# Kernel optimization log

Hardware: AMD Instinct MI355X
Metric: run time of the kernel (lower is better)

Reference implementation:

```python
import jax, jax.numpy as jnp
import numpy as np

B, D_IN, NQ, D_OUT = 65536, 1024, 64, 1024
PI = float(np.pi)


def setup_inputs() -> dict:
    key = jax.random.key(0)
    ks = jax.random.split(key, 6)
    return {
        "x": jax.random.normal(ks[0], (B, D_IN), dtype=jnp.float32),
        "W_in": jax.random.normal(ks[1], (NQ, D_IN), dtype=jnp.float32) * 0.02,
        "b_in": jax.random.normal(ks[2], (NQ,), dtype=jnp.float32) * 0.02,
        "quantum_params": jax.random.normal(ks[3], (NQ, 3), dtype=jnp.float32) * 0.1,
        "W_out": jax.random.normal(ks[4], (D_OUT, NQ), dtype=jnp.float32) * 0.02,
        "b_out": jax.random.normal(ks[5], (D_OUT,), dtype=jnp.float32) * 0.02,
    }


def reference(x, W_in, b_in, quantum_params, W_out, b_out):
    # input linear + tanh: [B, NQ]
    h = jnp.tanh(x @ W_in.T + b_in)
    # quantum forward, vectorized over (batch, qubit):
    # state = cos(h*pi/2)*cos(p0) + sin(p1)*cos(p2)
    angles = h * PI
    p0, p1, p2 = quantum_params[:, 0], quantum_params[:, 1], quantum_params[:, 2]
    state = jnp.cos(angles * 0.5) * jnp.cos(p0) + jnp.sin(p1) * jnp.cos(p2)
    # output linear: [B, D_OUT]
    return state @ W_out.T + b_out
```

## Files before the change

kernel.cpp:

```cpp
#include <hip/hip_runtime.h>
#include <hip/hip_bf16.h>
#include <math.h>

#define NB 65536
#define DIN 1024
#define NQ 64
#define DOUT 1024

typedef __attribute__((ext_vector_type(8))) short bf16x8;
typedef __attribute__((ext_vector_type(4))) float f32x4;

__device__ __forceinline__ unsigned short f2bf(float f) {
    union { float f; unsigned u; } v; v.f = f;
    unsigned r = (v.u + 0x7fffu + ((v.u >> 16) & 1u)) >> 16;
    return (unsigned short)r;
}

__global__ __launch_bounds__(256) void kP(const float* __restrict__ W_in,
                                          const float* __restrict__ W_out,
                                          const float* __restrict__ qp,
                                          unsigned short* __restrict__ Wb,
                                          unsigned short* __restrict__ Wob,
                                          float* __restrict__ cp0,
                                          float* __restrict__ cq) {
    int i = blockIdx.x * 256 + threadIdx.x;
    if (i < NQ * DIN)  Wb[i]  = f2bf(W_in[i]);
    if (i < DOUT * NQ) Wob[i] = f2bf(W_out[i]);
    if (i < NQ) {
        cp0[i] = cosf(qp[i * 3 + 0]);
        cq[i]  = sinf(qp[i * 3 + 1]) * cosf(qp[i * 3 + 2]);
    }
}

__global__ __launch_bounds__(256) void kA(const float* __restrict__ x,
                                          const unsigned short* __restrict__ Wb,
                                          const float* __restrict__ b_in,
                                          const float* __restrict__ cp0,
                                          const float* __restrict__ cq,
                                          unsigned short* __restrict__ state) {
    const int wave = threadIdx.x >> 6;
    const int lane = threadIdx.x & 63;
    const int r  = lane & 15;
    const int kg = lane >> 4;
    const int row0 = blockIdx.x * 64 + wave * 16;

    const float* xrow = x + (size_t)(row0 + r) * DIN + kg * 8;

    f32x4 acc[4] = {f32x4{0,0,0,0}, f32x4{0,0,0,0}, f32x4{0,0,0,0}, f32x4{0,0,0,0}};

    for (int k0 = 0; k0 < DIN; k0 += 32) {
        float4 a0 = *(const float4*)(xrow + k0);
        float4 a1 = *(const float4*)(xrow + k0 + 4);
        bf16x8 a;
        a[0] = (short)f2bf(a0.x); a[1] = (short)f2bf(a0.y);
        a[2] = (short)f2bf(a0.z); a[3] = (short)f2bf(a0.w);
        a[4] = (short)f2bf(a1.x); a[5] = (short)f2bf(a1.y);
        a[6] = (short)f2bf(a1.z); a[7] = (short)f2bf(a1.w);
        #pragma unroll
        for (int n = 0; n < 4; n++) {
            bf16x8 b = *(const bf16x8*)(Wb + (size_t)(n * 16 + r) * DIN + k0 + kg * 8);
            acc[n] = __builtin_amdgcn_mfma_f32_16x16x32_bf16(a, b, acc[n], 0, 0, 0);
        }
    }

    #pragma unroll
    for (int n = 0; n < 4; n++) {
        int q = n * 16 + r;
        float bi = b_in[q], c0 = cp0[q], c1 = cq[q];
        #pragma unroll
        for (int i = 0; i < 4; i++) {
            int row = row0 + kg * 4 + i;
            float h = tanhf(acc[n][i] + bi);
            float s = cosf(h * 1.57079632679489662f) * c0 + c1;
            state[(size_t)row * NQ + q] = f2bf(s);
        }
    }
}

__global__ __launch_bounds__(256) void kB(const unsigned short* __restrict__ state,
                                          const unsigned short* __restrict__ Wob,
                                          const float* __restrict__ b_out,
                                          float* __restrict__ out) {
    const int wave = threadIdx.x >> 6;
    const int lane = threadIdx.x & 63;
    const int r  = lane & 15;
    const int kg = lane >> 4;
    const int row0 = blockIdx.x * 16;
    const int n0 = wave * 256;

    const unsigned short* srow = state + (size_t)(row0 + r) * NQ + kg * 8;
    bf16x8 a0 = *(const bf16x8*)(srow);
    bf16x8 a1 = *(const bf16x8*)(srow + 32);

    f32x4 acc[16];
    #pragma unroll
    for (int n = 0; n < 16; n++) acc[n] = f32x4{0, 0, 0, 0};

    #pragma unroll
    for (int n = 0; n < 16; n++) {
        int col = n0 + n * 16 + r;
        const unsigned short* wp = Wob + (size_t)col * NQ + kg * 8;
        bf16x8 b0 = *(const bf16x8*)(wp);
        bf16x8 b1 = *(const bf16x8*)(wp + 32);
        acc[n] = __builtin_amdgcn_mfma_f32_16x16x32_bf16(a0, b0, acc[n], 0, 0, 0);
        acc[n] = __builtin_amdgcn_mfma_f32_16x16x32_bf16(a1, b1, acc[n], 0, 0, 0);
    }

    #pragma unroll
    for (int n = 0; n < 16; n++) {
        int col = n0 + n * 16 + r;
        float bo = b_out[col];
        #pragma unroll
        for (int i = 0; i < 4; i++) {
            out[(size_t)(row0 + kg * 4 + i) * DOUT + col] = acc[n][i] + bo;
        }
    }
}

extern "C" void kernel_launch(void* const* d_in, const int* in_sizes, int n_in,
                              void* d_out, int out_size, void* d_ws, size_t ws_size,
                              hipStream_t stream) {
    const float* x    = (const float*)d_in[0];
    const float* W_in = (const float*)d_in[1];
    const float* b_in = (const float*)d_in[2];
    const float* qp   = (const float*)d_in[3];
    const float* W_out= (const float*)d_in[4];
    const float* b_out= (const float*)d_in[5];
    float* out = (float*)d_out;

    char* ws = (char*)d_ws;
    unsigned short* Wb    = (unsigned short*)(ws);
    unsigned short* Wob   = (unsigned short*)(ws + 131072);
    float*          cp0   = (float*)(ws + 262144);
    float*          cq    = (float*)(ws + 262400);
    unsigned short* state = (unsigned short*)(ws + 1048576);

    kP<<<(NQ * DIN + 255) / 256, 256, 0, stream>>>(W_in, W_out, qp, Wb, Wob, cp0, cq);
    kA<<<NB / 64, 256, 0, stream>>>(x, Wb, b_in, cp0, cq, state);
    kB<<<NB / 16, 256, 0, stream>>>(state, Wob, b_out, out);
}
```

Baseline: 186.4 us.

## Fuse input and output GEMMs via LDS-staged state, use fast intrinsics

Result: slower. 208.9 us (+12.1%).

```diff
diff --git a/kernel.cpp b/kernel.cpp
--- a/kernel.cpp
+++ b/kernel.cpp
@@ -32,12 +32,16 @@
     }
 }
 
-__global__ __launch_bounds__(256) void kA(const float* __restrict__ x,
+__global__ __launch_bounds__(256) void kF(const float* __restrict__ x,
                                           const unsigned short* __restrict__ Wb,
                                           const float* __restrict__ b_in,
                                           const float* __restrict__ cp0,
                                           const float* __restrict__ cq,
-                                          unsigned short* __restrict__ state) {
+                                          const unsigned short* __restrict__ Wob,
+                                          const float* __restrict__ b_out,
+                                          float* __restrict__ out) {
+    __shared__ unsigned short st[4][16][72];
+
     const int wave = threadIdx.x >> 6;
     const int lane = threadIdx.x & 63;
     const int r  = lane & 15;
@@ -69,50 +73,44 @@
         float bi = b_in[q], c0 = cp0[q], c1 = cq[q];
         #pragma unroll
         for (int i = 0; i < 4; i++) {
-            int row = row0 + kg * 4 + i;
-            float h = tanhf(acc[n][i] + bi);
-            float s = cosf(h * 1.57079632679489662f) * c0 + c1;
-            state[(size_t)row * NQ + q] = f2bf(s);
+            float a  = acc[n][i] + bi;
+            float e2 = __builtin_amdgcn_exp2f(a * 2.8853900817779268f);
+            float th = 1.0f - 2.0f * __builtin_amdgcn_rcpf(e2 + 1.0f);
+            float s  = __builtin_amdgcn_cosf(th * 0.25f) * c0 + c1;
+            st[wave][kg * 4 + i][q] = f2bf(s);
         }
     }
-}
 
-__global__ __launch_bounds__(256) void kB(const unsigned short* __restrict__ state,
-                                          const unsigned short* __restrict__ Wob,
-                                          const float* __restrict__ b_out,
-                                          float* __restrict__ out) {
-    const int wave = threadIdx.x >> 6;
-    const int lane = threadIdx.x & 63;
-    const int r  = lane & 15;
-    const int kg = lane >> 4;
-    const int row0 = blockIdx.x * 16;
-    const int n0 = wave * 256;
+    __syncthreads();
 
-    const unsigned short* srow = state + (size_t)(row0 + r) * NQ + kg * 8;
-    bf16x8 a0 = *(const bf16x8*)(srow);
-    bf16x8 a1 = *(const bf16x8*)(srow + 32);
-
-    f32x4 acc[16];
-    #pragma unroll
-    for (int n = 0; n < 16; n++) acc[n] = f32x4{0, 0, 0, 0};
+    bf16x8 sa0 = *(const bf16x8*)&st[wave][r][kg * 8];
+    bf16x8 sa1 = *(const bf16x8*)&st[wave][r][32 + kg * 8];
 
     #pragma unroll
-    for (int n = 0; n < 16; n++) {
-        int col = n0 + n * 16 + r;
-        const unsigned short* wp = Wob + (size_t)col * NQ + kg * 8;
-        bf16x8 b0 = *(const bf16x8*)(wp);
-        bf16x8 b1 = *(const bf16x8*)(wp + 32);
-        acc[n] = __builtin_amdgcn_mfma_f32_16x16x32_bf16(a0, b0, acc[n], 0, 0, 0);
-        acc[n] = __builtin_amdgcn_mfma_f32_16x16x32_bf16(a1, b1, acc[n], 0, 0, 0);
-    }
+    for (int c = 0; c < 4; c++) {
+        f32x4 acc2[16];
+        #pragma unroll
+        for (int n = 0; n < 16; n++) acc2[n] = f32x4{0, 0, 0, 0};
 
-    #pragma unroll
-    for (int n = 0; n < 16; n++) {
-        int col = n0 + n * 16 + r;
-        float bo = b_out[col];
         #pragma unroll
-        for (int i = 0; i < 4; i++) {
-            out[(size_t)(row0 + kg * 4 + i) * DOUT + col] = acc[n][i] + bo;
+        for (int n = 0; n < 16; n++) {
+            int col = c * 256 + n * 16 + r;
+            const unsigned short* wp = Wob + (size_t)col * NQ + kg * 8;
+            bf16x8 b0 = *(const bf16x8*)(wp);
+            bf16x8 b1 = *(const bf16x8*)(wp + 32);
+            acc2[n] = __builtin_amdgcn_mfma_f32_16x16x32_bf16(sa0, b0, acc2[n], 0, 0, 0);
+            acc2[n] = __builtin_amdgcn_mfma_f32_16x16x32_bf16(sa1, b1, acc2[n], 0, 0, 0);
+        }
+
+        #pragma unroll
+        for (int n = 0; n < 16; n++) {
+            int col = c * 256 + n * 16 + r;
+            float bo = b_out[col];
+            #pragma unroll
+            for (int i = 0; i < 4; i++) {
+                __builtin_nontemporal_store(acc2[n][i] + bo,
+                    &out[(size_t)(row0 + kg * 4 + i) * DOUT + col]);
+            }
         }
     }
 }
@@ -129,13 +127,11 @@
     float* out = (float*)d_out;
 
     char* ws = (char*)d_ws;
-    unsigned short* Wb    = (unsigned short*)(ws);
-    unsigned short* Wob   = (unsigned short*)(ws + 131072);
-    float*          cp0   = (float*)(ws + 262144);
-    float*          cq    = (float*)(ws + 262400);
-    unsigned short* state = (unsigned short*)(ws + 1048576);
+    unsigned short* Wb  = (unsigned short*)(ws);
+    unsigned short* Wob = (unsigned short*)(ws + 131072);
+    float*          cp0 = (float*)(ws + 262144);
+    float*          cq  = (float*)(ws + 262400);
 
     kP<<<(NQ * DIN + 255) / 256, 256, 0, stream>>>(W_in, W_out, qp, Wb, Wob, cp0, cq);
-    kA<<<NB / 64, 256, 0, stream>>>(x, Wb, b_in, cp0, cq, state);
-    kB<<<NB / 16, 256, 0, stream>>>(state, Wob, b_out, out);
+    kF<<<NB / 64, 256, 0, stream>>>(x, Wb, b_in, cp0, cq, Wob, b_out, out);
 }
```
